# Optimization experiments

Measured on AMD Instinct MI355X. Metric: run time of the kernel, lower is better.

Reference implementation:

```python
import jax, jax.numpy as jnp
import numpy as np

B, L, D = 4, 1024, 1024
H, DK, DV = 16, 64, 64
TEMP = float(np.power(DK, 0.5))
LN_EPS = 1e-5


def setup_inputs() -> dict:
    key = jax.random.key(0)
    ks = jax.random.split(key, 11)
    s_qk = np.sqrt(2.0 / (D + DK))
    s_v = np.sqrt(2.0 / (D + DV))
    inp = {
        'q_in': jax.random.normal(ks[0], (B, L, D), jnp.float32),
        'k_in': jax.random.normal(ks[1], (B, L, D), jnp.float32),
        'v_in': jax.random.normal(ks[2], (B, L, D), jnp.float32),
        'Wq':  jax.random.normal(ks[3], (D, H * DK), jnp.float32) * s_qk,
        'Wq2': jax.random.normal(ks[4], (D, H * DK), jnp.float32) * s_qk,
        'Wk':  jax.random.normal(ks[5], (D, H * DK), jnp.float32) * s_qk,
        'Wv':  jax.random.normal(ks[6], (D, H * DV), jnp.float32) * s_v,
        'Wo':  jax.random.normal(ks[7], (H * DV, D), jnp.float32) * np.sqrt(2.0 / (H * DV + D)),
        'ln_g': jnp.ones((D,), jnp.float32),
        'ln_b': jnp.zeros((D,), jnp.float32),
        'Er':  jax.random.normal(ks[8], (H, L, DK), jnp.float32),
        # causal mask: True above the diagonal (positions to be masked with -inf)
        'mask': jnp.triu(jnp.ones((L, L), jnp.bool_), k=1)[None].repeat(B, axis=0),
    }
    return inp


def _skew(rel):
    # rel: [H, B, Lq, Lr] with Lr == Lq. Music-Transformer skew:
    # pad one zero column on the left, reshape, drop first row.
    h, b, lq, lr = rel.shape
    rel = jnp.pad(rel, ((0, 0), (0, 0), (0, 0), (1, 0)))        # [H,B,Lq,Lr+1]
    rel = rel.reshape(h, b, lr + 1, lq)                          # [H,B,Lr+1,Lq]
    return rel[:, :, 1:, :].reshape(h, b, lq, lr)                # [H,B,Lq,Lr]


def reference(q_in, k_in, v_in, Wq, Wq2, Wk, Wv, Wo, ln_g, ln_b, Er, mask):
    residual = q_in
    # projections -> [H, B, L, d]
    def proj(x, W, d):
        return x.reshape(B * L, D).dot(W).reshape(B, L, H, d).transpose(2, 0, 1, 3)
    q = proj(q_in, Wq, DK)
    q2 = proj(q_in, Wq2, DK)
    k = proj(k_in, Wk, DK)
    v = proj(v_in, Wv, DV)

    attn = jnp.einsum('hbqd,hbkd->hbqk', q, k) / TEMP            # [H,B,Lq,Lk]
    rel = _skew(jnp.einsum('hbqd,hrd->hbqr', q2, Er)) / TEMP     # [H,B,Lq,Lk]

    m = mask[None]                                               # [1,B,Lq,Lk]
    neg = jnp.float32(-jnp.inf)
    attn = jnp.where(m, neg, attn)
    rel = jnp.where(m, neg, rel)
    p = jax.nn.softmax(attn + rel, axis=-1)                      # [H,B,Lq,Lk]

    out = jnp.einsum('hbqk,hbkd->hbqd', p, v)                    # [H,B,Lq,DV]
    out = out.transpose(1, 2, 0, 3).reshape(B, L, H * DV)
    out = out.dot(Wo)                                            # dropout is identity (eval)

    x = out + residual
    mu = x.mean(-1, keepdims=True)
    var = x.var(-1, keepdims=True)
    y = (x - mu) * jax.lax.rsqrt(var + LN_EPS) * ln_g + ln_b
    return y, p
```

## Files before the change

### kernel.cpp

```cpp
#include <hip/hip_runtime.h>

typedef __bf16 bf16;
typedef __bf16 v8bf __attribute__((ext_vector_type(8)));
typedef float v4f __attribute__((ext_vector_type(4)));
typedef unsigned int v4u __attribute__((ext_vector_type(4)));

#define B_ 4
#define L_ 1024
#define D_ 1024
#define NEG (-3.0e38f)
#define MFMA16(a, b, c) __builtin_amdgcn_mfma_f32_16x16x32_bf16(a, b, c, 0, 0, 0)

typedef const __attribute__((address_space(1))) void* gas_t;
typedef __attribute__((address_space(3))) void* las_t;
__device__ __forceinline__ void gl_lds16(const bf16* g, bf16* l)
{
    __builtin_amdgcn_global_load_lds((gas_t)g, (las_t)l, 16, 0, 0);
}

__global__ __launch_bounds__(256) void wconv_kernel(
    const float* __restrict__ w0, const float* __restrict__ w1,
    const float* __restrict__ w2, const float* __restrict__ w3,
    const float* __restrict__ w4, const float* __restrict__ er,
    const float* __restrict__ qin, const float* __restrict__ kin,
    const float* __restrict__ vin,
    bf16* __restrict__ wt, bf16* __restrict__ erb,
    bf16* __restrict__ qbf, bf16* __restrict__ kbf, bf16* __restrict__ vbf)
{
    int z = blockIdx.z;
    int tx = threadIdx.x, ty = threadIdx.y;
    if (z < 5) {
        const float* src = z == 0 ? w0 : z == 1 ? w1 : z == 2 ? w2 : z == 3 ? w3 : w4;
        bf16* dst = wt + (size_t)z * 1024 * 1024;
        __shared__ float t[32][33];
        int bx = blockIdx.x * 32, by = blockIdx.y * 32;
#pragma unroll
        for (int i = 0; i < 4; i++)
            t[ty + i * 8][tx] = src[(size_t)(by + ty + i * 8) * 1024 + bx + tx];
        __syncthreads();
#pragma unroll
        for (int i = 0; i < 4; i++)
            dst[(size_t)(bx + ty + i * 8) * 1024 + by + tx] = (bf16)t[tx][ty + i * 8];
    } else if (z == 5) {
        int base = (blockIdx.y * 32 + blockIdx.x) * 256 + ty * 32 + tx;
#pragma unroll
        for (int i = 0; i < 4; i++) {
            int idx = base + i * 262144;
            erb[idx] = (bf16)er[idx];
        }
    } else {
        const float* src = z == 6 ? qin : z == 7 ? kin : vin;
        bf16* dst = z == 6 ? qbf : z == 7 ? kbf : vbf;
        int id = (blockIdx.y * 32 + blockIdx.x) * 256 + ty * 32 + tx;
#pragma unroll
        for (int i = 0; i < 4; i++) {
            int j = id * 4 + i * 1048576;
            float4 v = *(const float4*)(src + j);
            union { bf16 h[4]; uint2 u; } t;
            t.h[0] = (bf16)v.x; t.h[1] = (bf16)v.y;
            t.h[2] = (bf16)v.z; t.h[3] = (bf16)v.w;
            *(uint2*)(dst + j) = t.u;
        }
    }
}

__global__ __launch_bounds__(256) void gemm64(
    const bf16* __restrict__ Ab, const bf16* __restrict__ Bt,
    float* __restrict__ Cf, bf16* __restrict__ Cb, bf16* __restrict__ Cb2,
    int K, int mode)
{
    __shared__ __align__(16) bf16 As[2][64 * 32];
    __shared__ __align__(16) bf16 Bs[2][128 * 32];
    int tid = threadIdx.x, lane = tid & 63, w = tid >> 6;
    int tn = blockIdx.x * 128, tm = blockIdx.y * 64;
    int wn = w * 32;
    int m15 = lane & 15, rq = lane >> 4, kq = rq * 8;

    v4f acc[4][2];
#pragma unroll
    for (int m = 0; m < 4; ++m)
#pragma unroll
        for (int n = 0; n < 2; ++n)
#pragma unroll
            for (int i = 0; i < 4; ++i) acc[m][n][i] = 0.f;

    int sr = lane >> 2, sc8 = (lane & 3) * 8;
    const bf16* ga  = Ab + (size_t)(tm + w * 16 + sr) * K + sc8;
    const bf16* gb0 = Bt + (size_t)(tn + w * 32 + sr) * K + sc8;
    const bf16* gb1 = gb0 + (size_t)16 * K;

#define GSTAGE(buf, k0s) { \
    gl_lds16(ga  + (k0s), As[buf] + w * 16 * 32); \
    gl_lds16(gb0 + (k0s), Bs[buf] + w * 32 * 32); \
    gl_lds16(gb1 + (k0s), Bs[buf] + (w * 32 + 16) * 32); }

    int cur = 0;
    GSTAGE(0, 0);
    __syncthreads();
    for (int k0 = 0; k0 < K; k0 += 32) {
        if (k0 + 32 < K) GSTAGE(cur ^ 1, k0 + 32);
        v8bf a[4], bb[2];
#pragma unroll
        for (int m = 0; m < 4; ++m)
            a[m] = *(const v8bf*)&As[cur][(m * 16 + m15) * 32 + kq];
#pragma unroll
        for (int n = 0; n < 2; ++n)
            bb[n] = *(const v8bf*)&Bs[cur][(wn + n * 16 + m15) * 32 + kq];
#pragma unroll
        for (int m = 0; m < 4; ++m)
#pragma unroll
            for (int n = 0; n < 2; ++n)
                acc[m][n] = MFMA16(a[m], bb[n], acc[m][n]);
        __syncthreads();
        cur ^= 1;
    }
#undef GSTAGE

#pragma unroll
    for (int m = 0; m < 4; ++m)
#pragma unroll
        for (int n = 0; n < 2; ++n) {
            int col = tn + wn + n * 16 + m15;
            if (mode == 2) {
                union { bf16 h[4]; uint2 u; } pk;
#pragma unroll
                for (int i = 0; i < 4; ++i) pk.h[i] = (bf16)acc[m][n][i];
                int row0 = tm + m * 16 + rq * 4;
                int bb2 = row0 >> 10, l = row0 & 1023, hh = col >> 6, dv = col & 63;
                *(uint2*)&Cb[(((size_t)(bb2 * 16 + hh) * 64 + dv) << 10) + l] = pk.u;
            } else {
#pragma unroll
                for (int i = 0; i < 4; ++i) {
                    int row = tm + m * 16 + rq * 4 + i;
                    float v = acc[m][n][i];
                    if (mode == 1) Cf[(size_t)row * 1024 + col] = v;
                    else {
                        bf16* dst = col < 1024 ? Cb : Cb2;
                        dst[(size_t)row * 1024 + (col & 1023)] = (bf16)v;
                    }
                }
            }
        }
}

__global__ __launch_bounds__(256, 4) void attn_mfma(
    const bf16* __restrict__ qb, const bf16* __restrict__ q2b,
    const bf16* __restrict__ kb, const bf16* __restrict__ vt,
    const bf16* __restrict__ erb, float* __restrict__ p_out,
    bf16* __restrict__ ab)
{
    int lin = blockIdx.x;
    int bh  = (lin & 7) | ((lin >> 6) << 3);
    int pp  = (lin >> 3) & 7;
    int h = bh >> 2, b = bh & 3;
    int tid = threadIdx.x, lane = tid & 63, w = tid >> 6;
    int m15 = lane & 15, rq = lane >> 4, kq = rq * 8;
    int li0 = w * 16 + rq * 4;

    __shared__ float RELs[64][68];

    size_t pb = (size_t)(h * 4 + b) << 20;
    size_t kbase = ((size_t)(b << 10) * 16 + h) * 64;
    size_t vbase = ((size_t)(b * 16 + h) << 16);
    const bf16* erh = erb + ((size_t)h << 16);

    for (int qs = 0; qs < 2; ++qs) {
        int qt = qs ? pp : 15 - pp;
        int q0 = qt << 6, nkt = qt + 1, t0 = 15 - qt;

        {
            int zr = tid >> 2, zc = (tid & 3) * 16;
            v4f zz = {0.f, 0.f, 0.f, 0.f};
            for (int kt = qt + 1; kt < 16; ++kt) {
                float* basep = p_out + pb + ((size_t)(q0 + zr) << 10) + kt * 64 + zc;
#pragma unroll
                for (int i = 0; i < 4; ++i)
                    __builtin_nontemporal_store(zz, (v4f*)(basep + i * 4));
            }
        }

        const bf16* qrow  = &qb [((size_t)((b << 10) + q0 + w * 16 + m15) * 16 + h) * 64];
        const bf16* q2row = &q2b[((size_t)((b << 10) + q0 + w * 16 + m15) * 16 + h) * 64];
        v8bf alo  = *(const v8bf*)(qrow + kq);
        v8bf ahi  = *(const v8bf*)(qrow + kq + 32);
        v8bf a2lo = *(const v8bf*)(q2row + kq);
        v8bf a2hi = *(const v8bf*)(q2row + kq + 32);

        float m_run[4], l_run[4], linv[4];
#pragma unroll
        for (int i = 0; i < 4; ++i) { m_run[i] = NEG; l_run[i] = 0.f; }
        v4f oacc[4];
#pragma unroll
        for (int t = 0; t < 4; ++t)
#pragma unroll
            for (int i = 0; i < 4; ++i) oacc[t][i] = 0.f;

        for (int pass = 0; pass < 2; ++pass) {
            if (pass) {
#pragma unroll
                for (int i = 0; i < 4; ++i) linv[i] = 1.f / l_run[i];
            }
            for (int kt = 0; kt < nkt; ++kt) {
                int k0 = kt << 6, tA = t0 + kt;
                bool hasB = tA < 15;
                const bf16* eA = erh + ((size_t)tA << 12);

                __builtin_amdgcn_s_setprio(1);
#pragma unroll
                for (int ct = 0; ct < 4; ++ct) {
                    const bf16* er_ = eA + (ct * 16 + m15) * 64;
                    v4f a4 = {0.f, 0.f, 0.f, 0.f};
                    a4 = MFMA16(a2lo, *(const v8bf*)(er_ + kq), a4);
                    a4 = MFMA16(a2hi, *(const v8bf*)(er_ + kq + 32), a4);
                    int c = ct * 16 + m15;
#pragma unroll
                    for (int i = 0; i < 4; ++i) {
                        int kl = c + li0 + i - 63;
                        if (kl >= 0) RELs[li0 + i][kl] = a4[i];
                    }
                }
                if (hasB) {
                    const bf16* eB = eA + 4096;
#pragma unroll
                    for (int ct = 0; ct < 4; ++ct) {
                        const bf16* er_ = eB + (ct * 16 + m15) * 64;
                        v4f a4 = {0.f, 0.f, 0.f, 0.f};
                        a4 = MFMA16(a2lo, *(const v8bf*)(er_ + kq), a4);
                        a4 = MFMA16(a2hi, *(const v8bf*)(er_ + kq + 32), a4);
                        int c = ct * 16 + m15;
#pragma unroll
                        for (int i = 0; i < 4; ++i) {
                            int kl = c + li0 + i + 1;
                            if (kl < 64) RELs[li0 + i][kl] = a4[i];
                        }
                    }
                }
                v4f qk[4];
#pragma unroll
                for (int ct = 0; ct < 4; ++ct) {
                    const bf16* kr = kb + kbase + (size_t)(k0 + ct * 16 + m15) * 1024;
                    v4f a4 = {0.f, 0.f, 0.f, 0.f};
                    a4 = MFMA16(alo, *(const v8bf*)(kr + kq), a4);
                    qk[ct] = MFMA16(ahi, *(const v8bf*)(kr + kq + 32), a4);
                }
                __builtin_amdgcn_s_setprio(0);

                float sc[4][4];
#pragma unroll
                for (int ct = 0; ct < 4; ++ct)
#pragma unroll
                    for (int i = 0; i < 4; ++i) {
                        int li = li0 + i;
                        int j = ct * 16 + m15;
                        float v = (qk[ct][i] + RELs[li][j]) * 0.125f;
                        if (!hasB) v = (j > li) ? NEG : v;
                        sc[ct][i] = v;
                    }
                if (!pass) {
#pragma unroll
                    for (int i = 0; i < 4; ++i) {
                        float tmax = fmaxf(fmaxf(sc[0][i], sc[1][i]), fmaxf(sc[2][i], sc[3][i]));
#pragma unroll
                        for (int off = 1; off < 16; off <<= 1)
                            tmax = fmaxf(tmax, __shfl_xor(tmax, off));
                        float mn = fmaxf(m_run[i], tmax);
                        float es = __expf(sc[0][i] - mn) + __expf(sc[1][i] - mn)
                                 + __expf(sc[2][i] - mn) + __expf(sc[3][i] - mn);
#pragma unroll
                        for (int off = 1; off < 16; off <<= 1)
                            es += __shfl_xor(es, off);
                        l_run[i] = l_run[i] * __expf(m_run[i] - mn) + es;
                        m_run[i] = mn;
                    }
                } else {
#pragma unroll
                    for (int ct = 0; ct < 4; ++ct)
#pragma unroll
                        for (int i = 0; i < 4; ++i) {
                            int li = li0 + i;
                            int j = ct * 16 + m15;
                            RELs[li][j] = __expf(sc[ct][i] - m_run[i]) * linv[i];
                        }
                    asm volatile("" ::: "memory");
#pragma unroll
                    for (int i2 = 0; i2 < 2; ++i2)
#pragma unroll
                        for (int jh = 0; jh < 2; ++jh) {
                            int rr = w * 16 + (lane >> 3) + 8 * i2;
                            v4u val = *(const v4u*)((const char*)&RELs[rr][0]
                                                    + (lane & 7) * 16 + 128 * jh);
                            __builtin_nontemporal_store(val,
                                (v4u*)(p_out + pb + ((size_t)(q0 + rr) << 10) + k0
                                       + (lane & 7) * 4 + 32 * jh));
                        }
                    const float* pr = &RELs[w * 16 + m15][0];
                    v4f f0 = *(const v4f*)(pr + kq);
                    v4f f1 = *(const v4f*)(pr + kq + 4);
                    v4f f2 = *(const v4f*)(pr + kq + 32);
                    v4f f3 = *(const v4f*)(pr + kq + 36);
                    v8bf plo, phi;
#pragma unroll
                    for (int j = 0; j < 4; ++j) {
                        plo[j] = (bf16)f0[j]; plo[j + 4] = (bf16)f1[j];
                        phi[j] = (bf16)f2[j]; phi[j + 4] = (bf16)f3[j];
                    }
                    __builtin_amdgcn_s_setprio(1);
#pragma unroll
                    for (int ct = 0; ct < 4; ++ct) {
                        const bf16* vr = vt + vbase + (size_t)(ct * 16 + m15) * 1024 + k0;
                        oacc[ct] = MFMA16(plo, *(const v8bf*)(vr + kq), oacc[ct]);
                        oacc[ct] = MFMA16(phi, *(const v8bf*)(vr + kq + 32), oacc[ct]);
                    }
                    __builtin_amdgcn_s_setprio(0);
                }
            }
        }

#pragma unroll
        for (int ct = 0; ct < 4; ++ct)
#pragma unroll
            for (int i = 0; i < 4; ++i)
                ab[((size_t)((b << 10) + q0 + li0 + i) * 16 + h) * 64 + ct * 16 + m15] =
                    (bf16)oacc[ct][i];
    }
}

__global__ __launch_bounds__(256) void ln_kernel(
    const float* __restrict__ y0, const float* __restrict__ res,
    const float* __restrict__ g, const float* __restrict__ bb,
    float* __restrict__ y)
{
    int row = blockIdx.x, tid = threadIdx.x, lane = tid & 63, w = tid >> 6;
    __shared__ float rs[4], rq2[4];
    const float* xr = y0 + (size_t)row * D_;
    const float* rr = res + (size_t)row * D_;
    float x[4], sum = 0.f, sq = 0.f;
#pragma unroll
    for (int i = 0; i < 4; i++) {
        int c = tid + i * 256;
        x[i] = xr[c] + rr[c];
        sum += x[i]; sq += x[i] * x[i];
    }
#pragma unroll
    for (int off = 32; off; off >>= 1) { sum += __shfl_xor(sum, off); sq += __shfl_xor(sq, off); }
    if (lane == 0) { rs[w] = sum; rq2[w] = sq; }
    __syncthreads();
    sum = rs[0] + rs[1] + rs[2] + rs[3];
    sq  = rq2[0] + rq2[1] + rq2[2] + rq2[3];
    float mean = sum * (1.f / D_);
    float var  = sq * (1.f / D_) - mean * mean;
    float inv  = rsqrtf(var + 1e-5f);
#pragma unroll
    for (int i = 0; i < 4; i++) {
        int c = tid + i * 256;
        y[(size_t)row * D_ + c] = (x[i] - mean) * inv * g[c] + bb[c];
    }
}

extern "C" void kernel_launch(void* const* d_in, const int* in_sizes, int n_in,
                              void* d_out, int out_size, void* d_ws, size_t ws_size,
                              hipStream_t stream)
{
    const float* q_in = (const float*)d_in[0];
    const float* k_in = (const float*)d_in[1];
    const float* v_in = (const float*)d_in[2];
    const float* Wq   = (const float*)d_in[3];
    const float* Wq2  = (const float*)d_in[4];
    const float* Wk   = (const float*)d_in[5];
    const float* Wv   = (const float*)d_in[6];
    const float* Wo   = (const float*)d_in[7];
    const float* ln_g = (const float*)d_in[8];
    const float* ln_b = (const float*)d_in[9];
    const float* Er   = (const float*)d_in[10];

    float* y_out = (float*)d_out;
    float* p_out = y_out + (size_t)B_ * L_ * D_;

    char* ws = (char*)d_ws;
    const size_t MB = 1024 * 1024;
    bf16*  wT  = (bf16*)(ws);
    bf16*  erb = (bf16*)(ws + 10 * MB);
    bf16*  qb  = (bf16*)(ws + 12 * MB);
    bf16*  q2b = (bf16*)(ws + 20 * MB);
    bf16*  kb  = (bf16*)(ws + 28 * MB);
    bf16*  vtb = (bf16*)(ws + 36 * MB);
    bf16*  ab  = (bf16*)(ws + 44 * MB);
    float* y0  = (float*)(ws + 52 * MB);

    bf16* qbf = (bf16*)((char*)p_out + 160 * MB);
    bf16* kbf = (bf16*)((char*)p_out + 168 * MB);
    bf16* vbf = (bf16*)((char*)p_out + 176 * MB);

    wconv_kernel<<<dim3(32, 32, 9), dim3(32, 8), 0, stream>>>(
        Wq, Wq2, Wk, Wv, Wo, Er, q_in, k_in, v_in, wT, erb, qbf, kbf, vbf);

    gemm64<<<dim3(16, 64), 256, 0, stream>>>(qbf, wT,          nullptr, qb,  q2b,     1024, 0);
    gemm64<<<dim3( 8, 64), 256, 0, stream>>>(kbf, wT + 2 * MB, nullptr, kb,  nullptr, 1024, 0);
    gemm64<<<dim3( 8, 64), 256, 0, stream>>>(vbf, wT + 3 * MB, nullptr, vtb, nullptr, 1024, 2);

    attn_mfma<<<dim3(512), dim3(256), 0, stream>>>(qb, q2b, kb, vtb, erb, p_out, ab);

    gemm64<<<dim3( 8, 64), 256, 0, stream>>>(ab, wT + 4 * MB, y0, nullptr, nullptr, 1024, 1);
    ln_kernel<<<4096, 256, 0, stream>>>(y0, q_in, ln_g, ln_b, y_out);
}
```

Baseline: 668.9 us.

## Fuse Q/K/V projection GEMMs into one launch and split attention blocks per q-tile

The three projection GEMMs are merged into a single kernel whose blocks pick the Q, K or V problem by blockIdx.x, removing two launches and letting all projection tiles share one wave. The attention kernel no longer pairs two q-tiles (qt and 15-qt) per block for load balance; it launches 1024 blocks with one q-tile each, ordered largest-first. This gives more parallelism and less per-block serial work, but drops the explicit pairing that balanced the causal workload.

Measured after the change: 793.6 us. +18.6%, slower.

```diff
diff --git a/kernel.cpp b/kernel.cpp
--- a/kernel.cpp
+++ b/kernel.cpp
@@ -64,15 +64,13 @@
     }
 }
 
-__global__ __launch_bounds__(256) void gemm64(
+__device__ __forceinline__ void gemm_core(
     const bf16* __restrict__ Ab, const bf16* __restrict__ Bt,
     float* __restrict__ Cf, bf16* __restrict__ Cb, bf16* __restrict__ Cb2,
-    int K, int mode)
-{
-    __shared__ __align__(16) bf16 As[2][64 * 32];
-    __shared__ __align__(16) bf16 Bs[2][128 * 32];
+    int K, int mode, int tn, int tm,
+    bf16* __restrict__ As , bf16* __restrict__ Bs )
+{
     int tid = threadIdx.x, lane = tid & 63, w = tid >> 6;
-    int tn = blockIdx.x * 128, tm = blockIdx.y * 64;
     int wn = w * 32;
     int m15 = lane & 15, rq = lane >> 4, kq = rq * 8;
 
@@ -90,9 +88,9 @@
     const bf16* gb1 = gb0 + (size_t)16 * K;
 
 #define GSTAGE(buf, k0s) { \
-    gl_lds16(ga  + (k0s), As[buf] + w * 16 * 32); \
-    gl_lds16(gb0 + (k0s), Bs[buf] + w * 32 * 32); \
-    gl_lds16(gb1 + (k0s), Bs[buf] + (w * 32 + 16) * 32); }
+    gl_lds16(ga  + (k0s), As + (buf) * 64 * 32 + w * 16 * 32); \
+    gl_lds16(gb0 + (k0s), Bs + (buf) * 128 * 32 + w * 32 * 32); \
+    gl_lds16(gb1 + (k0s), Bs + (buf) * 128 * 32 + (w * 32 + 16) * 32); }
 
     int cur = 0;
     GSTAGE(0, 0);
@@ -102,10 +100,10 @@
         v8bf a[4], bb[2];
 #pragma unroll
         for (int m = 0; m < 4; ++m)
-            a[m] = *(const v8bf*)&As[cur][(m * 16 + m15) * 32 + kq];
+            a[m] = *(const v8bf*)&As[cur * 64 * 32 + (m * 16 + m15) * 32 + kq];
 #pragma unroll
         for (int n = 0; n < 2; ++n)
-            bb[n] = *(const v8bf*)&Bs[cur][(wn + n * 16 + m15) * 32 + kq];
+            bb[n] = *(const v8bf*)&Bs[cur * 128 * 32 + (wn + n * 16 + m15) * 32 + kq];
 #pragma unroll
         for (int m = 0; m < 4; ++m)
 #pragma unroll
@@ -143,6 +141,37 @@
         }
 }
 
+__global__ __launch_bounds__(256) void gemm_proj(
+    const bf16* __restrict__ qbf, const bf16* __restrict__ kbf,
+    const bf16* __restrict__ vbf, const bf16* __restrict__ wT,
+    bf16* __restrict__ qb, bf16* __restrict__ q2b,
+    bf16* __restrict__ kb, bf16* __restrict__ vtb)
+{
+    __shared__ __align__(16) bf16 As[2][64 * 32];
+    __shared__ __align__(16) bf16 Bs[2][128 * 32];
+    int bx = blockIdx.x, tm = blockIdx.y * 64;
+    const size_t MB = 1024 * 1024;
+    if (bx < 16)
+        gemm_core(qbf, wT, nullptr, qb, q2b, 1024, 0, bx * 128, tm,
+                  &As[0][0], &Bs[0][0]);
+    else if (bx < 24)
+        gemm_core(kbf, wT + 2 * MB, nullptr, kb, nullptr, 1024, 0,
+                  (bx - 16) * 128, tm, &As[0][0], &Bs[0][0]);
+    else
+        gemm_core(vbf, wT + 3 * MB, nullptr, vtb, nullptr, 1024, 2,
+                  (bx - 24) * 128, tm, &As[0][0], &Bs[0][0]);
+}
+
+__global__ __launch_bounds__(256) void gemm_out(
+    const bf16* __restrict__ ab, const bf16* __restrict__ woT,
+    float* __restrict__ y0)
+{
+    __shared__ __align__(16) bf16 As[2][64 * 32];
+    __shared__ __align__(16) bf16 Bs[2][128 * 32];
+    gemm_core(ab, woT, y0, nullptr, nullptr, 1024, 1,
+              blockIdx.x * 128, blockIdx.y * 64, &As[0][0], &Bs[0][0]);
+}
+
 __global__ __launch_bounds__(256, 4) void attn_mfma(
     const bf16* __restrict__ qb, const bf16* __restrict__ q2b,
     const bf16* __restrict__ kb, const bf16* __restrict__ vt,
@@ -150,9 +179,10 @@
     bf16* __restrict__ ab)
 {
     int lin = blockIdx.x;
-    int bh  = (lin & 7) | ((lin >> 6) << 3);
-    int pp  = (lin >> 3) & 7;
+    int bh  = lin & 63;
+    int qt  = 15 - (lin >> 6);
     int h = bh >> 2, b = bh & 3;
+    int q0 = qt << 6, nkt = qt + 1, t0 = 15 - qt;
     int tid = threadIdx.x, lane = tid & 63, w = tid >> 6;
     int m15 = lane & 15, rq = lane >> 4, kq = rq * 8;
     int li0 = w * 16 + rq * 4;
@@ -164,165 +194,160 @@
     size_t vbase = ((size_t)(b * 16 + h) << 16);
     const bf16* erh = erb + ((size_t)h << 16);
 
-    for (int qs = 0; qs < 2; ++qs) {
-        int qt = qs ? pp : 15 - pp;
-        int q0 = qt << 6, nkt = qt + 1, t0 = 15 - qt;
-
-        {
-            int zr = tid >> 2, zc = (tid & 3) * 16;
-            v4f zz = {0.f, 0.f, 0.f, 0.f};
-            for (int kt = qt + 1; kt < 16; ++kt) {
-                float* basep = p_out + pb + ((size_t)(q0 + zr) << 10) + kt * 64 + zc;
-#pragma unroll
-                for (int i = 0; i < 4; ++i)
-                    __builtin_nontemporal_store(zz, (v4f*)(basep + i * 4));
+    {
+        int zr = tid >> 2, zc = (tid & 3) * 16;
+        v4f zz = {0.f, 0.f, 0.f, 0.f};
+        for (int kt = qt + 1; kt < 16; ++kt) {
+            float* basep = p_out + pb + ((size_t)(q0 + zr) << 10) + kt * 64 + zc;
+#pragma unroll
+            for (int i = 0; i < 4; ++i)
+                __builtin_nontemporal_store(zz, (v4f*)(basep + i * 4));
+        }
+    }
+
+    const bf16* qrow  = &qb [((size_t)((b << 10) + q0 + w * 16 + m15) * 16 + h) * 64];
+    const bf16* q2row = &q2b[((size_t)((b << 10) + q0 + w * 16 + m15) * 16 + h) * 64];
+    v8bf alo  = *(const v8bf*)(qrow + kq);
+    v8bf ahi  = *(const v8bf*)(qrow + kq + 32);
+    v8bf a2lo = *(const v8bf*)(q2row + kq);
+    v8bf a2hi = *(const v8bf*)(q2row + kq + 32);
+
+    float m_run[4], l_run[4], linv[4];
+#pragma unroll
+    for (int i = 0; i < 4; ++i) { m_run[i] = NEG; l_run[i] = 0.f; }
+    v4f oacc[4];
+#pragma unroll
+    for (int t = 0; t < 4; ++t)
+#pragma unroll
+        for (int i = 0; i < 4; ++i) oacc[t][i] = 0.f;
+
+    for (int pass = 0; pass < 2; ++pass) {
+        if (pass) {
+#pragma unroll
+            for (int i = 0; i < 4; ++i) linv[i] = 1.f / l_run[i];
+        }
+        for (int kt = 0; kt < nkt; ++kt) {
+            int k0 = kt << 6, tA = t0 + kt;
+            bool hasB = tA < 15;
+            const bf16* eA = erh + ((size_t)tA << 12);
+
+            __builtin_amdgcn_s_setprio(1);
+#pragma unroll
+            for (int ct = 0; ct < 4; ++ct) {
+                const bf16* er_ = eA + (ct * 16 + m15) * 64;
+                v4f a4 = {0.f, 0.f, 0.f, 0.f};
+                a4 = MFMA16(a2lo, *(const v8bf*)(er_ + kq), a4);
+                a4 = MFMA16(a2hi, *(const v8bf*)(er_ + kq + 32), a4);
+                int c = ct * 16 + m15;
+#pragma unroll
+                for (int i = 0; i < 4; ++i) {
+                    int kl = c + li0 + i - 63;
+                    if (kl >= 0) RELs[li0 + i][kl] = a4[i];
+                }
             }
-        }
-
-        const bf16* qrow  = &qb [((size_t)((b << 10) + q0 + w * 16 + m15) * 16 + h) * 64];
-        const bf16* q2row = &q2b[((size_t)((b << 10) + q0 + w * 16 + m15) * 16 + h) * 64];
-        v8bf alo  = *(const v8bf*)(qrow + kq);
-        v8bf ahi  = *(const v8bf*)(qrow + kq + 32);
-        v8bf a2lo = *(const v8bf*)(q2row + kq);
-        v8bf a2hi = *(const v8bf*)(q2row + kq + 32);
-
-        float m_run[4], l_run[4], linv[4];
-#pragma unroll
-        for (int i = 0; i < 4; ++i) { m_run[i] = NEG; l_run[i] = 0.f; }
-        v4f oacc[4];
-#pragma unroll
-        for (int t = 0; t < 4; ++t)
-#pragma unroll
-            for (int i = 0; i < 4; ++i) oacc[t][i] = 0.f;
-
-        for (int pass = 0; pass < 2; ++pass) {
-            if (pass) {
-#pragma unroll
-                for (int i = 0; i < 4; ++i) linv[i] = 1.f / l_run[i];
-            }
-            for (int kt = 0; kt < nkt; ++kt) {
-                int k0 = kt << 6, tA = t0 + kt;
-                bool hasB = tA < 15;
-                const bf16* eA = erh + ((size_t)tA << 12);
-
-                __builtin_amdgcn_s_setprio(1);
+            if (hasB) {
+                const bf16* eB = eA + 4096;
 #pragma unroll
                 for (int ct = 0; ct < 4; ++ct) {
-                    const bf16* er_ = eA + (ct * 16 + m15) * 64;
+                    const bf16* er_ = eB + (ct * 16 + m15) * 64;
                     v4f a4 = {0.f, 0.f, 0.f, 0.f};
                     a4 = MFMA16(a2lo, *(const v8bf*)(er_ + kq), a4);
                     a4 = MFMA16(a2hi, *(const v8bf*)(er_ + kq + 32), a4);
                     int c = ct * 16 + m15;
 #pragma unroll
                     for (int i = 0; i < 4; ++i) {
-                        int kl = c + li0 + i - 63;
-                        if (kl >= 0) RELs[li0 + i][kl] = a4[i];
+                        int kl = c + li0 + i + 1;
+                        if (kl < 64) RELs[li0 + i][kl] = a4[i];
                     }
                 }
-                if (hasB) {
-                    const bf16* eB = eA + 4096;
-#pragma unroll
-                    for (int ct = 0; ct < 4; ++ct) {
-                        const bf16* er_ = eB + (ct * 16 + m15) * 64;
-                        v4f a4 = {0.f, 0.f, 0.f, 0.f};
-                        a4 = MFMA16(a2lo, *(const v8bf*)(er_ + kq), a4);
-                        a4 = MFMA16(a2hi, *(const v8bf*)(er_ + kq + 32), a4);
-                        int c = ct * 16 + m15;
-#pragma unroll
-                        for (int i = 0; i < 4; ++i) {
-                            int kl = c + li0 + i + 1;
-                            if (kl < 64) RELs[li0 + i][kl] = a4[i];
-                        }
-                    }
-                }
-                v4f qk[4];
-#pragma unroll
-                for (int ct = 0; ct < 4; ++ct) {
-                    const bf16* kr = kb + kbase + (size_t)(k0 + ct * 16 + m15) * 1024;
-                    v4f a4 = {0.f, 0.f, 0.f, 0.f};
-                    a4 = MFMA16(alo, *(const v8bf*)(kr + kq), a4);
-                    qk[ct] = MFMA16(ahi, *(const v8bf*)(kr + kq + 32), a4);
-                }
-                __builtin_amdgcn_s_setprio(0);
-
-                float sc[4][4];
+            }
+            v4f qk[4];
+#pragma unroll
+            for (int ct = 0; ct < 4; ++ct) {
+                const bf16* kr = kb + kbase + (size_t)(k0 + ct * 16 + m15) * 1024;
+                v4f a4 = {0.f, 0.f, 0.f, 0.f};
+                a4 = MFMA16(alo, *(const v8bf*)(kr + kq), a4);
+                qk[ct] = MFMA16(ahi, *(const v8bf*)(kr + kq + 32), a4);
+            }
+            __builtin_amdgcn_s_setprio(0);
+
+            float sc[4][4];
+#pragma unroll
+            for (int ct = 0; ct < 4; ++ct)
+#pragma unroll
+                for (int i = 0; i < 4; ++i) {
+                    int li = li0 + i;
+                    int j = ct * 16 + m15;
+                    float v = (qk[ct][i] + RELs[li][j]) * 0.125f;
+                    if (!hasB) v = (j > li) ? NEG : v;
+                    sc[ct][i] = v;
+                }
+            if (!pass) {
+#pragma unroll
+                for (int i = 0; i < 4; ++i) {
+                    float tmax = fmaxf(fmaxf(sc[0][i], sc[1][i]), fmaxf(sc[2][i], sc[3][i]));
+#pragma unroll
+                    for (int off = 1; off < 16; off <<= 1)
+                        tmax = fmaxf(tmax, __shfl_xor(tmax, off));
+                    float mn = fmaxf(m_run[i], tmax);
+                    float es = __expf(sc[0][i] - mn) + __expf(sc[1][i] - mn)
+                             + __expf(sc[2][i] - mn) + __expf(sc[3][i] - mn);
+#pragma unroll
+                    for (int off = 1; off < 16; off <<= 1)
+                        es += __shfl_xor(es, off);
+                    l_run[i] = l_run[i] * __expf(m_run[i] - mn) + es;
+                    m_run[i] = mn;
+                }
+            } else {
 #pragma unroll
                 for (int ct = 0; ct < 4; ++ct)
 #pragma unroll
                     for (int i = 0; i < 4; ++i) {
                         int li = li0 + i;
                         int j = ct * 16 + m15;
-                        float v = (qk[ct][i] + RELs[li][j]) * 0.125f;
-                        if (!hasB) v = (j > li) ? NEG : v;
-                        sc[ct][i] = v;
+                        RELs[li][j] = __expf(sc[ct][i] - m_run[i]) * linv[i];
                     }
-                if (!pass) {
-#pragma unroll
-                    for (int i = 0; i < 4; ++i) {
-                        float tmax = fmaxf(fmaxf(sc[0][i], sc[1][i]), fmaxf(sc[2][i], sc[3][i]));
-#pragma unroll
-                        for (int off = 1; off < 16; off <<= 1)
-                            tmax = fmaxf(tmax, __shfl_xor(tmax, off));
-                        float mn = fmaxf(m_run[i], tmax);
-                        float es = __expf(sc[0][i] - mn) + __expf(sc[1][i] - mn)
-                                 + __expf(sc[2][i] - mn) + __expf(sc[3][i] - mn);
-#pragma unroll
-                        for (int off = 1; off < 16; off <<= 1)
-                            es += __shfl_xor(es, off);
-                        l_run[i] = l_run[i] * __expf(m_run[i] - mn) + es;
-                        m_run[i] = mn;
+                asm volatile("" ::: "memory");
+#pragma unroll
+                for (int i2 = 0; i2 < 2; ++i2)
+#pragma unroll
+                    for (int jh = 0; jh < 2; ++jh) {
+                        int rr = w * 16 + (lane >> 3) + 8 * i2;
+                        v4u val = *(const v4u*)((const char*)&RELs[rr][0]
+                                                + (lane & 7) * 16 + 128 * jh);
+                        __builtin_nontemporal_store(val,
+                            (v4u*)(p_out + pb + ((size_t)(q0 + rr) << 10) + k0
+                                   + (lane & 7) * 4 + 32 * jh));
                     }
-                } else {
-#pragma unroll
-                    for (int ct = 0; ct < 4; ++ct)
-#pragma unroll
-                        for (int i = 0; i < 4; ++i) {
-                            int li = li0 + i;
-                            int j = ct * 16 + m15;
-                            RELs[li][j] = __expf(sc[ct][i] - m_run[i]) * linv[i];
-                        }
-                    asm volatile("" ::: "memory");
-#pragma unroll
-                    for (int i2 = 0; i2 < 2; ++i2)
-#pragma unroll
-                        for (int jh = 0; jh < 2; ++jh) {
-                            int rr = w * 16 + (lane >> 3) + 8 * i2;
-                            v4u val = *(const v4u*)((const char*)&RELs[rr][0]
-                                                    + (lane & 7) * 16 + 128 * jh);
-                            __builtin_nontemporal_store(val,
-                                (v4u*)(p_out + pb + ((size_t)(q0 + rr) << 10) + k0
-                                       + (lane & 7) * 4 + 32 * jh));
-                        }
-                    const float* pr = &RELs[w * 16 + m15][0];
-                    v4f f0 = *(const v4f*)(pr + kq);
-                    v4f f1 = *(const v4f*)(pr + kq + 4);
-                    v4f f2 = *(const v4f*)(pr + kq + 32);
-                    v4f f3 = *(const v4f*)(pr + kq + 36);
-                    v8bf plo, phi;
-#pragma unroll
-                    for (int j = 0; j < 4; ++j) {
-                        plo[j] = (bf16)f0[j]; plo[j + 4] = (bf16)f1[j];
-                        phi[j] = (bf16)f2[j]; phi[j + 4] = (bf16)f3[j];
-                    }
-                    __builtin_amdgcn_s_setprio(1);
-#pragma unroll
-                    for (int ct = 0; ct < 4; ++ct) {
-                        const bf16* vr = vt + vbase + (size_t)(ct * 16 + m15) * 1024 + k0;
-                        oacc[ct] = MFMA16(plo, *(const v8bf*)(vr + kq), oacc[ct]);
-                        oacc[ct] = MFMA16(phi, *(const v8bf*)(vr + kq + 32), oacc[ct]);
-                    }
-                    __builtin_amdgcn_s_setprio(0);
-                }
+                const float* pr = &RELs[w * 16 + m15][0];
+                v4f f0 = *(const v4f*)(pr + kq);
+                v4f f1 = *(const v4f*)(pr + kq + 4);
+                v4f f2 = *(const v4f*)(pr + kq + 32);
+                v4f f3 = *(const v4f*)(pr + kq + 36);
+                v8bf plo, phi;
+#pragma unroll
+                for (int j = 0; j < 4; ++j) {
+                    plo[j] = (bf16)f0[j]; plo[j + 4] = (bf16)f1[j];
+                    phi[j] = (bf16)f2[j]; phi[j + 4] = (bf16)f3[j];
+                }
+                __builtin_amdgcn_s_setprio(1);
+#pragma unroll
+                for (int ct = 0; ct < 4; ++ct) {
+                    const bf16* vr = vt + vbase + (size_t)(ct * 16 + m15) * 1024 + k0;
+                    oacc[ct] = MFMA16(plo, *(const v8bf*)(vr + kq), oacc[ct]);
+                    oacc[ct] = MFMA16(phi, *(const v8bf*)(vr + kq + 32), oacc[ct]);
+                }
+                __builtin_amdgcn_s_setprio(0);
             }
         }
-
-#pragma unroll
-        for (int ct = 0; ct < 4; ++ct)
-#pragma unroll
-            for (int i = 0; i < 4; ++i)
-                ab[((size_t)((b << 10) + q0 + li0 + i) * 16 + h) * 64 + ct * 16 + m15] =
-                    (bf16)oacc[ct][i];
-    }
+    }
+
+#pragma unroll
+    for (int ct = 0; ct < 4; ++ct)
+#pragma unroll
+        for (int i = 0; i < 4; ++i)
+            ab[((size_t)((b << 10) + q0 + li0 + i) * 16 + h) * 64 + ct * 16 + m15] =
+                (bf16)oacc[ct][i];
 }
 
 __global__ __launch_bounds__(256) void ln_kernel(
@@ -394,12 +419,11 @@
     wconv_kernel<<<dim3(32, 32, 9), dim3(32, 8), 0, stream>>>(
         Wq, Wq2, Wk, Wv, Wo, Er, q_in, k_in, v_in, wT, erb, qbf, kbf, vbf);
 
-    gemm64<<<dim3(16, 64), 256, 0, stream>>>(qbf, wT,          nullptr, qb,  q2b,     1024, 0);
-    gemm64<<<dim3( 8, 64), 256, 0, stream>>>(kbf, wT + 2 * MB, nullptr, kb,  nullptr, 1024, 0);
-    gemm64<<<dim3( 8, 64), 256, 0, stream>>>(vbf, wT + 3 * MB, nullptr, vtb, nullptr, 1024, 2);
-
-    attn_mfma<<<dim3(512), dim3(256), 0, stream>>>(qb, q2b, kb, vtb, erb, p_out, ab);
-
-    gemm64<<<dim3( 8, 64), 256, 0, stream>>>(ab, wT + 4 * MB, y0, nullptr, nullptr, 1024, 1);
+    gemm_proj<<<dim3(32, 64), 256, 0, stream>>>(qbf, kbf, vbf, wT,
+                                                qb, q2b, kb, vtb);
+
+    attn_mfma<<<dim3(1024), dim3(256), 0, stream>>>(qb, q2b, kb, vtb, erb, p_out, ab);
+
+    gemm_out<<<dim3(8, 64), 256, 0, stream>>>(ab, wT + 4 * MB, y0);
     ln_kernel<<<4096, 256, 0, stream>>>(y0, q_in, ln_g, ln_b, y_out);
 }
```
